# Kernel optimization log

Hardware: AMD Instinct MI355X
Metric: run time of the kernel (lower is better)

The kernel has to match this reference:

```python
import jax, jax.numpy as jnp
import numpy as np

D = 256          # in_dim == out_dim for both layers
B, S = 8, 1024   # batch, seq_len
EPS = 1e-5       # LayerNorm eps (torch default)


def _layernorm(x, g, b):
    mu = jnp.mean(x, axis=-1, keepdims=True)
    var = jnp.var(x, axis=-1, keepdims=True)
    return (x - mu) * jax.lax.rsqrt(var + EPS) * g + b


def _periods(d):
    i = jnp.arange(d, dtype=jnp.float32)
    # periods[i, j] = i*d + j + 2
    return i[:, None] * d + i[None, :] + 2.0


def _layer(x, M, P, g, b, positions):
    # x: [B, S, in_dim] -> [B, S, out_dim]
    x_trans = jnp.einsum('bsj,ij->bsi', x, M)      # x @ M.T
    x_trans = _layernorm(x_trans, g, b)
    k = positions.astype(jnp.float32)[:, None, None]            # [S,1,1]
    phi = jnp.cos(2.0 * jnp.pi * k / _periods(D)[None])         # [S,D,D]
    Mk = P[None] * phi                                          # [S,D,D]
    Nk = jnp.einsum('bsj,sij->bsi', x_trans, Mk)
    # use_residual='separate' with in_dim==out_dim -> Identity residual
    return Nk + x


def setup_inputs() -> dict:
    key = jax.random.key(0)
    ks = jax.random.split(key, 5)
    seq = jax.random.normal(ks[0], (B, S, D), dtype=jnp.float32)
    M1 = jax.random.uniform(ks[1], (D, D), jnp.float32, -0.5, 0.5)
    P1 = jax.random.uniform(ks[2], (D, D), jnp.float32, -0.1, 0.1)
    M2 = jax.random.uniform(ks[3], (D, D), jnp.float32, -0.5, 0.5)
    P2 = jax.random.uniform(ks[4], (D, D), jnp.float32, -0.1, 0.1)
    g1 = jnp.ones((D,), jnp.float32); b1 = jnp.zeros((D,), jnp.float32)
    g2 = jnp.ones((D,), jnp.float32); b2 = jnp.zeros((D,), jnp.float32)
    return {"seq": seq, "M1": M1, "P1": P1, "g1": g1, "b1": b1,
            "M2": M2, "P2": P2, "g2": g2, "b2": b2}


def reference(seq, M1, P1, g1, b1, M2, P2, g2, b2):
    positions = jnp.arange(S)
    x = _layer(seq, M1, P1, g1, b1, positions)
    x = _layer(x, M2, P2, g2, b2, positions)
    return x
```

## Files before the change

### kernel.cpp

```cpp
#include <hip/hip_runtime.h>

#define DD 256
#define BB 8
#define SS 1024
#define XSTRIDE 264
#define RSTRIDE 260

#define LAYER_BYTES 262144
#define PTAB_OFF    131072
#define WS_NEEDED   (2 * LAYER_BYTES)

typedef _Float16 half8  __attribute__((ext_vector_type(8)));
typedef _Float16 half2t __attribute__((ext_vector_type(2)));
typedef __fp16   fp16x2 __attribute__((ext_vector_type(2)));
typedef __attribute__((ext_vector_type(4))) float float4v;

union h8u { half8 h; half2t h2[4]; };

__device__ __forceinline__ half2t pkrtz(float a, float b) {
    union { fp16x2 f; half2t h; } cv;
    cv.f = __builtin_amdgcn_cvt_pkrtz(a, b);
    return cv.h;
}

__device__ __forceinline__ float cosrev(float x) {
    return __builtin_amdgcn_cosf(__builtin_amdgcn_fractf(x));
}
__device__ __forceinline__ float cosq(float x) {
    return __builtin_amdgcn_cosf(x);
}

__global__ void build_tabs(const float* __restrict__ M1, const float* __restrict__ P1,
                           const float* __restrict__ M2, const float* __restrict__ P2,
                           char* __restrict__ ws)
{
    int gid   = blockIdx.x * 256 + threadIdx.x;
    int layer = gid >> 13;
    int gi    = gid & 8191;
    int idx   = gi >> 6;
    int lane  = gi & 63;
    int wt    = idx & 15;
    int l15   = lane & 15, quad = lane >> 4;
    int kt    = idx >> 4;
    int n     = 16 * wt + l15;
    int j0    = kt * 32 + quad * 8;

    const float* Msrc = layer ? M2 : M1;
    const float* Psrc = layer ? P2 : P1;

    h8u mh, ph;
    #pragma unroll
    for (int e = 0; e < 4; ++e) {
        float ma = Msrc[(size_t)n * DD + j0 + 2 * e];
        float mb = Msrc[(size_t)n * DD + j0 + 2 * e + 1];
        float pa = Psrc[(size_t)n * DD + j0 + 2 * e];
        float pb = Psrc[(size_t)n * DD + j0 + 2 * e + 1];
        mh.h2[e] = pkrtz(ma, mb);
        ph.h2[e] = pkrtz(pa, pb);
    }
    char* base = ws + (size_t)layer * LAYER_BYTES;
    ((half8*)base)[gi]              = mh.h;
    ((half8*)(base + PTAB_OFF))[gi] = ph.h;
}

template<bool TABS>
__global__ __launch_bounds__(512, 8)
void fused_hierddpm(const float* __restrict__ seq,
                    const float* __restrict__ M1, const float* __restrict__ P1,
                    const float* __restrict__ g1, const float* __restrict__ be1,
                    const float* __restrict__ M2, const float* __restrict__ P2,
                    const float* __restrict__ g2, const float* __restrict__ be2,
                    const char* __restrict__ ws,
                    float* __restrict__ out)
{
    __shared__ __align__(16) _Float16 xsb[8][XSTRIDE];
    __shared__ __align__(16) _Float16 xtb[8][XSTRIDE];
    __shared__ __align__(16) float2 stats[8][8];
    __shared__ __align__(16) float res_lds[8][RSTRIDE];

    const int tid  = threadIdx.x;
    const int w    = tid >> 6;
    const int lane = tid & 63;
    const int l15  = lane & 15;
    const int l7   = l15 & 7;
    const int quad = lane >> 4;
    const int s    = blockIdx.x;
    const float k0 = (float)s;

    {
        const float4* seq4 = (const float4*)seq;
        int row = tid >> 6, j4 = tid & 63;
        float4 x = seq4[((size_t)row * SS + s) * 64 + j4];
        half2t* dst = (half2t*)&xsb[row][4 * j4];
        dst[0] = pkrtz(x.x, x.y);
        dst[1] = pkrtz(x.z, x.w);
        *(float4*)&res_lds[row][4 * j4] = x;
    }
    __syncthreads();

    #pragma unroll 1
    for (int layer = 0; layer < 2; ++layer) {
        const float* M  = layer ? M2  : M1;
        const float* P  = layer ? P2  : P1;
        const float* g  = layer ? g2  : g1;
        const float* be = layer ? be2 : be1;
        const char*  lbase = ws + (size_t)layer * LAYER_BYTES;
        const half8* Mtab = (const half8*)lbase;
        const half8* Ptab = (const half8*)(lbase + PTAB_OFF);

        float4v acc1[2];
        acc1[0] = (float4v){0.f, 0.f, 0.f, 0.f};
        acc1[1] = (float4v){0.f, 0.f, 0.f, 0.f};

        #pragma unroll 1
        for (int kt = 0; kt < 8; ++kt) {
            half8 a = *(const half8*)&xsb[l7][kt * 32 + quad * 8];
            #pragma unroll
            for (int t = 0; t < 2; ++t) {
                half8 bf;
                if (TABS) {
                    bf = Mtab[(kt * 16 + 2 * w + t) * 64 + lane];
                } else {
                    int n = 16 * (2 * w + t) + l15;
                    const float4* Mr = (const float4*)M + ((size_t)n * 64 + kt * 8 + quad * 2);
                    float4 m0 = Mr[0], m1 = Mr[1];
                    h8u bb2;
                    bb2.h2[0] = pkrtz(m0.x, m0.y);
                    bb2.h2[1] = pkrtz(m0.z, m0.w);
                    bb2.h2[2] = pkrtz(m1.x, m1.y);
                    bb2.h2[3] = pkrtz(m1.z, m1.w);
                    bf = bb2.h;
                }
                acc1[t] = __builtin_amdgcn_mfma_f32_16x16x32_f16(a, bf, acc1[t], 0, 0, 0);
            }
        }

        #pragma unroll
        for (int reg = 0; reg < 4; ++reg) {
            float v0 = acc1[0][reg], v1 = acc1[1][reg];
            float sm = v0 + v1;
            float sq = fmaf(v0, v0, v1 * v1);
            #pragma unroll
            for (int off = 1; off < 16; off <<= 1) {
                sm += __shfl_xor(sm, off, 64);
                sq += __shfl_xor(sq, off, 64);
            }
            if (l15 == 0 && quad < 2) stats[quad * 4 + reg][w] = make_float2(sm, sq);
        }
        __syncthreads();
        if (quad < 2) {
            int c0i = 16 * (2 * w) + l15, c1i = c0i + 16;
            float gv0 = g[c0i], bv0 = be[c0i];
            float gv1 = g[c1i], bv1 = be[c1i];
            #pragma unroll
            for (int reg = 0; reg < 4; ++reg) {
                int m = quad * 4 + reg;
                const float4* s4 = (const float4*)&stats[m][0];
                float4 q0 = s4[0], q1 = s4[1], q2 = s4[2], q3 = s4[3];
                float sm = (q0.x + q0.z) + (q1.x + q1.z) + (q2.x + q2.z) + (q3.x + q3.z);
                float sq = (q0.y + q0.w) + (q1.y + q1.w) + (q2.y + q2.w) + (q3.y + q3.w);
                float mm = sm * (1.f / DD);
                float rs = rsqrtf(sq * (1.f / DD) - mm * mm + 1e-5f);
                xtb[m][c0i] = (_Float16)fmaf((acc1[0][reg] - mm) * rs, gv0, bv0);
                xtb[m][c1i] = (_Float16)fmaf((acc1[1][reg] - mm) * rs, gv1, bv1);
            }
        }
        __syncthreads();

        float4v accS[2];
        accS[0] = (float4v){0.f, 0.f, 0.f, 0.f};
        accS[1] = (float4v){0.f, 0.f, 0.f, 0.f};

        float fb0 = (float)((16 * (2 * w) + l15) * DD + quad * 8 + 2);
        float fb1 = fb0 + 16.0f * DD;

        #pragma unroll 1
        for (int kt = 0; kt < 8; ++kt) {
            half8 a = *(const half8*)&xtb[l7][kt * 32 + quad * 8];
            {
                h8u pC;
                if (TABS) {
                    pC.h = Ptab[(kt * 16 + 2 * w) * 64 + lane];
                } else {
                    int n = 16 * (2 * w) + l15;
                    const float4* Pr = (const float4*)P + ((size_t)n * 64 + kt * 8 + quad * 2);
                    float4 p0 = Pr[0], p1 = Pr[1];
                    pC.h2[0] = pkrtz(p0.x, p0.y);
                    pC.h2[1] = pkrtz(p0.z, p0.w);
                    pC.h2[2] = pkrtz(p1.x, p1.y);
                    pC.h2[3] = pkrtz(p1.z, p1.w);
                }
                h8u bA;
                if (w == 0) {
                    #pragma unroll
                    for (int e = 0; e < 4; ++e) {
                        float ia = __builtin_amdgcn_rcpf(fb0 + (float)(2 * e));
                        float ib = __builtin_amdgcn_rcpf(fb0 + (float)(2 * e + 1));
                        bA.h2[e] = pC.h2[e] * pkrtz(cosrev(k0 * ia), cosrev(k0 * ib));
                    }
                } else {
                    #pragma unroll
                    for (int e = 0; e < 4; ++e) {
                        float ia = __builtin_amdgcn_rcpf(fb0 + (float)(2 * e));
                        float ib = __builtin_amdgcn_rcpf(fb0 + (float)(2 * e + 1));
                        bA.h2[e] = pC.h2[e] * pkrtz(cosq(k0 * ia), cosq(k0 * ib));
                    }
                }
                accS[0] = __builtin_amdgcn_mfma_f32_16x16x32_f16(a, bA.h, accS[0], 0, 0, 0);
                fb0 += 32.0f;
            }
            {
                h8u pC;
                if (TABS) {
                    pC.h = Ptab[(kt * 16 + 2 * w + 1) * 64 + lane];
                } else {
                    int n = 16 * (2 * w + 1) + l15;
                    const float4* Pr = (const float4*)P + ((size_t)n * 64 + kt * 8 + quad * 2);
                    float4 p0 = Pr[0], p1 = Pr[1];
                    pC.h2[0] = pkrtz(p0.x, p0.y);
                    pC.h2[1] = pkrtz(p0.z, p0.w);
                    pC.h2[2] = pkrtz(p1.x, p1.y);
                    pC.h2[3] = pkrtz(p1.z, p1.w);
                }
                h8u bB;
                #pragma unroll
                for (int e = 0; e < 4; ++e) {
                    float ia = __builtin_amdgcn_rcpf(fb1 + (float)(2 * e));
                    float ib = __builtin_amdgcn_rcpf(fb1 + (float)(2 * e + 1));
                    bB.h2[e] = pC.h2[e] * pkrtz(cosq(k0 * ia), cosq(k0 * ib));
                }
                accS[1] = __builtin_amdgcn_mfma_f32_16x16x32_f16(a, bB.h, accS[1], 0, 0, 0);
                fb1 += 32.0f;
            }
        }

        if (quad < 2) {
            #pragma unroll
            for (int t = 0; t < 2; ++t) {
                int col = 16 * (2 * w + t) + l15;
                #pragma unroll
                for (int reg = 0; reg < 4; ++reg) {
                    int m = quad * 4 + reg;
                    float val = accS[t][reg] + res_lds[m][col];
                    if (layer == 0) {
                        res_lds[m][col] = val;
                        xsb[m][col] = (_Float16)val;
                    } else {
                        out[((size_t)m * SS + s) * DD + col] = val;
                    }
                }
            }
        }
        if (layer == 0) __syncthreads();
    }
}

extern "C" void kernel_launch(void* const* d_in, const int* in_sizes, int n_in,
                              void* d_out, int out_size, void* d_ws, size_t ws_size,
                              hipStream_t stream)
{
    const float* seq = (const float*)d_in[0];
    const float* M1  = (const float*)d_in[1];
    const float* P1  = (const float*)d_in[2];
    const float* g1  = (const float*)d_in[3];
    const float* b1  = (const float*)d_in[4];
    const float* M2  = (const float*)d_in[5];
    const float* P2  = (const float*)d_in[6];
    const float* g2  = (const float*)d_in[7];
    const float* b2  = (const float*)d_in[8];
    float* out = (float*)d_out;

    if (ws_size >= WS_NEEDED) {
        build_tabs<<<64, 256, 0, stream>>>(M1, P1, M2, P2, (char*)d_ws);
        fused_hierddpm<true><<<SS, 512, 0, stream>>>(
            seq, M1, P1, g1, b1, M2, P2, g2, b2, (const char*)d_ws, out);
    } else {
        fused_hierddpm<false><<<SS, 512, 0, stream>>>(
            seq, M1, P1, g1, b1, M2, P2, g2, b2, nullptr, out);
    }
}
```

Measured before the change: 116.5 us.

## Precompute reciprocal period table and software-pipeline table loads in both GEMM loops

The prep kernel now also writes a float table of 1/period values for each layer, so the main kernel loads reciprocals instead of computing rcp on the fly. Both the M GEMM loop and the P-phase loop are double-buffered: next-iteration LDS and global table loads are issued before the current MFMAs. The first P/I tile loads are hoisted above the LayerNorm stats phase to hide latency. This trades rcp ALU work for extra global memory traffic (32 bytes per lane per tile) and higher register pressure, which could reduce occupancy under the 512x8 launch bounds.

```diff
diff --git a/kernel.cpp b/kernel.cpp
--- a/kernel.cpp
+++ b/kernel.cpp
@@ -6,8 +6,9 @@
 #define XSTRIDE 264
 #define RSTRIDE 260
 
-#define LAYER_BYTES 262144
+#define LAYER_BYTES 524288
 #define PTAB_OFF    131072
+#define ITAB_OFF    262144
 #define WS_NEEDED   (2 * LAYER_BYTES)
 
 typedef _Float16 half8  __attribute__((ext_vector_type(8)));
@@ -49,6 +50,7 @@
     const float* Psrc = layer ? P2 : P1;
 
     h8u mh, ph;
+    float iv[8];
     #pragma unroll
     for (int e = 0; e < 4; ++e) {
         float ma = Msrc[(size_t)n * DD + j0 + 2 * e];
@@ -57,10 +59,15 @@
         float pb = Psrc[(size_t)n * DD + j0 + 2 * e + 1];
         mh.h2[e] = pkrtz(ma, mb);
         ph.h2[e] = pkrtz(pa, pb);
+        iv[2 * e]     = 1.0f / (float)(n * DD + j0 + 2 * e + 2);
+        iv[2 * e + 1] = 1.0f / (float)(n * DD + j0 + 2 * e + 3);
     }
     char* base = ws + (size_t)layer * LAYER_BYTES;
     ((half8*)base)[gi]              = mh.h;
     ((half8*)(base + PTAB_OFF))[gi] = ph.h;
+    float4* it = (float4*)(base + ITAB_OFF);
+    it[2 * gi]     = make_float4(iv[0], iv[1], iv[2], iv[3]);
+    it[2 * gi + 1] = make_float4(iv[4], iv[5], iv[6], iv[7]);
 }
 
 template<bool TABS>
@@ -105,22 +112,35 @@
         const float* g  = layer ? g2  : g1;
         const float* be = layer ? be2 : be1;
         const char*  lbase = ws + (size_t)layer * LAYER_BYTES;
-        const half8* Mtab = (const half8*)lbase;
-        const half8* Ptab = (const half8*)(lbase + PTAB_OFF);
+        const half8*  Mtab = (const half8*)lbase;
+        const half8*  Ptab = (const half8*)(lbase + PTAB_OFF);
+        const float4* Itab = (const float4*)(lbase + ITAB_OFF);
 
         float4v acc1[2];
         acc1[0] = (float4v){0.f, 0.f, 0.f, 0.f};
         acc1[1] = (float4v){0.f, 0.f, 0.f, 0.f};
 
-        #pragma unroll 1
-        for (int kt = 0; kt < 8; ++kt) {
-            half8 a = *(const half8*)&xsb[l7][kt * 32 + quad * 8];
-            #pragma unroll
-            for (int t = 0; t < 2; ++t) {
-                half8 bf;
-                if (TABS) {
-                    bf = Mtab[(kt * 16 + 2 * w + t) * 64 + lane];
-                } else {
+        if (TABS) {
+            half8 aN  = *(const half8*)&xsb[l7][quad * 8];
+            half8 b0N = Mtab[(2 * w) * 64 + lane];
+            half8 b1N = Mtab[(2 * w + 1) * 64 + lane];
+            #pragma unroll 1
+            for (int kt = 0; kt < 8; ++kt) {
+                half8 aC = aN, b0C = b0N, b1C = b1N;
+                if (kt < 7) {
+                    aN  = *(const half8*)&xsb[l7][(kt + 1) * 32 + quad * 8];
+                    b0N = Mtab[((kt + 1) * 16 + 2 * w) * 64 + lane];
+                    b1N = Mtab[((kt + 1) * 16 + 2 * w + 1) * 64 + lane];
+                }
+                acc1[0] = __builtin_amdgcn_mfma_f32_16x16x32_f16(aC, b0C, acc1[0], 0, 0, 0);
+                acc1[1] = __builtin_amdgcn_mfma_f32_16x16x32_f16(aC, b1C, acc1[1], 0, 0, 0);
+            }
+        } else {
+            #pragma unroll 1
+            for (int kt = 0; kt < 8; ++kt) {
+                half8 a = *(const half8*)&xsb[l7][kt * 32 + quad * 8];
+                #pragma unroll
+                for (int t = 0; t < 2; ++t) {
                     int n = 16 * (2 * w + t) + l15;
                     const float4* Mr = (const float4*)M + ((size_t)n * 64 + kt * 8 + quad * 2);
                     float4 m0 = Mr[0], m1 = Mr[1];
@@ -129,10 +149,18 @@
                     bb2.h2[1] = pkrtz(m0.z, m0.w);
                     bb2.h2[2] = pkrtz(m1.x, m1.y);
                     bb2.h2[3] = pkrtz(m1.z, m1.w);
-                    bf = bb2.h;
-                }
-                acc1[t] = __builtin_amdgcn_mfma_f32_16x16x32_f16(a, bf, acc1[t], 0, 0, 0);
-            }
+                    acc1[t] = __builtin_amdgcn_mfma_f32_16x16x32_f16(a, bb2.h, acc1[t], 0, 0, 0);
+                }
+            }
+        }
+
+        half8 p0N, p1N;
+        float4 i0aN, i0bN, i1aN, i1bN;
+        if (TABS) {
+            int g0 = (2 * w) * 64 + lane, g1i = (2 * w + 1) * 64 + lane;
+            p0N = Ptab[g0];             p1N = Ptab[g1i];
+            i0aN = Itab[2 * g0];        i0bN = Itab[2 * g0 + 1];
+            i1aN = Itab[2 * g1i];       i1bN = Itab[2 * g1i + 1];
         }
 
         #pragma unroll
@@ -171,66 +199,75 @@
         accS[0] = (float4v){0.f, 0.f, 0.f, 0.f};
         accS[1] = (float4v){0.f, 0.f, 0.f, 0.f};
 
-        float fb0 = (float)((16 * (2 * w) + l15) * DD + quad * 8 + 2);
-        float fb1 = fb0 + 16.0f * DD;
-
-        #pragma unroll 1
-        for (int kt = 0; kt < 8; ++kt) {
-            half8 a = *(const half8*)&xtb[l7][kt * 32 + quad * 8];
-            {
-                h8u pC;
-                if (TABS) {
-                    pC.h = Ptab[(kt * 16 + 2 * w) * 64 + lane];
-                } else {
-                    int n = 16 * (2 * w) + l15;
+        if (TABS) {
+            half8 aN = *(const half8*)&xtb[l7][quad * 8];
+            #pragma unroll 1
+            for (int kt = 0; kt < 8; ++kt) {
+                half8 aC = aN;
+                h8u p0C, p1C;
+                p0C.h = p0N; p1C.h = p1N;
+                float4 i0a = i0aN, i0b = i0bN, i1a = i1aN, i1b = i1bN;
+                if (kt < 7) {
+                    int g0 = ((kt + 1) * 16 + 2 * w) * 64 + lane;
+                    int g1i = ((kt + 1) * 16 + 2 * w + 1) * 64 + lane;
+                    aN  = *(const half8*)&xtb[l7][(kt + 1) * 32 + quad * 8];
+                    p0N = Ptab[g0];        p1N = Ptab[g1i];
+                    i0aN = Itab[2 * g0];   i0bN = Itab[2 * g0 + 1];
+                    i1aN = Itab[2 * g1i];  i1bN = Itab[2 * g1i + 1];
+                }
+                {
+                    float iv[8] = {i0a.x, i0a.y, i0a.z, i0a.w, i0b.x, i0b.y, i0b.z, i0b.w};
+                    h8u bA;
+                    if (w == 0) {
+                        #pragma unroll
+                        for (int e = 0; e < 4; ++e)
+                            bA.h2[e] = p0C.h2[e] * pkrtz(cosrev(k0 * iv[2 * e]),
+                                                         cosrev(k0 * iv[2 * e + 1]));
+                    } else {
+                        #pragma unroll
+                        for (int e = 0; e < 4; ++e)
+                            bA.h2[e] = p0C.h2[e] * pkrtz(cosq(k0 * iv[2 * e]),
+                                                         cosq(k0 * iv[2 * e + 1]));
+                    }
+                    accS[0] = __builtin_amdgcn_mfma_f32_16x16x32_f16(aC, bA.h, accS[0], 0, 0, 0);
+                }
+                {
+                    float iv[8] = {i1a.x, i1a.y, i1a.z, i1a.w, i1b.x, i1b.y, i1b.z, i1b.w};
+                    h8u bB;
+                    #pragma unroll
+                    for (int e = 0; e < 4; ++e)
+                        bB.h2[e] = p1C.h2[e] * pkrtz(cosq(k0 * iv[2 * e]),
+                                                     cosq(k0 * iv[2 * e + 1]));
+                    accS[1] = __builtin_amdgcn_mfma_f32_16x16x32_f16(aC, bB.h, accS[1], 0, 0, 0);
+                }
+            }
+        } else {
+            float fb0 = (float)((16 * (2 * w) + l15) * DD + quad * 8 + 2);
+            float fb1 = fb0 + 16.0f * DD;
+            #pragma unroll 1
+            for (int kt = 0; kt < 8; ++kt) {
+                half8 a = *(const half8*)&xtb[l7][kt * 32 + quad * 8];
+                #pragma unroll
+                for (int t = 0; t < 2; ++t) {
+                    int n = 16 * (2 * w + t) + l15;
                     const float4* Pr = (const float4*)P + ((size_t)n * 64 + kt * 8 + quad * 2);
                     float4 p0 = Pr[0], p1 = Pr[1];
+                    h8u pC;
                     pC.h2[0] = pkrtz(p0.x, p0.y);
                     pC.h2[1] = pkrtz(p0.z, p0.w);
                     pC.h2[2] = pkrtz(p1.x, p1.y);
                     pC.h2[3] = pkrtz(p1.z, p1.w);
-                }
-                h8u bA;
-                if (w == 0) {
+                    float fb = (t == 0) ? fb0 : fb1;
+                    h8u bA;
                     #pragma unroll
                     for (int e = 0; e < 4; ++e) {
-                        float ia = __builtin_amdgcn_rcpf(fb0 + (float)(2 * e));
-                        float ib = __builtin_amdgcn_rcpf(fb0 + (float)(2 * e + 1));
+                        float ia = __builtin_amdgcn_rcpf(fb + (float)(2 * e));
+                        float ib = __builtin_amdgcn_rcpf(fb + (float)(2 * e + 1));
                         bA.h2[e] = pC.h2[e] * pkrtz(cosrev(k0 * ia), cosrev(k0 * ib));
                     }
-                } else {
-                    #pragma unroll
-                    for (int e = 0; e < 4; ++e) {
-                        float ia = __builtin_amdgcn_rcpf(fb0 + (float)(2 * e));
-                        float ib = __builtin_amdgcn_rcpf(fb0 + (float)(2 * e + 1));
-                        bA.h2[e] = pC.h2[e] * pkrtz(cosq(k0 * ia), cosq(k0 * ib));
-                    }
-                }
-                accS[0] = __builtin_amdgcn_mfma_f32_16x16x32_f16(a, bA.h, accS[0], 0, 0, 0);
-                fb0 += 32.0f;
-            }
-            {
-                h8u pC;
-                if (TABS) {
-                    pC.h = Ptab[(kt * 16 + 2 * w + 1) * 64 + lane];
-                } else {
-                    int n = 16 * (2 * w + 1) + l15;
-                    const float4* Pr = (const float4*)P + ((size_t)n * 64 + kt * 8 + quad * 2);
-                    float4 p0 = Pr[0], p1 = Pr[1];
-                    pC.h2[0] = pkrtz(p0.x, p0.y);
-                    pC.h2[1] = pkrtz(p0.z, p0.w);
-                    pC.h2[2] = pkrtz(p1.x, p1.y);
-                    pC.h2[3] = pkrtz(p1.z, p1.w);
-                }
-                h8u bB;
-                #pragma unroll
-                for (int e = 0; e < 4; ++e) {
-                    float ia = __builtin_amdgcn_rcpf(fb1 + (float)(2 * e));
-                    float ib = __builtin_amdgcn_rcpf(fb1 + (float)(2 * e + 1));
-                    bB.h2[e] = pC.h2[e] * pkrtz(cosq(k0 * ia), cosq(k0 * ib));
-                }
-                accS[1] = __builtin_amdgcn_mfma_f32_16x16x32_f16(a, bB.h, accS[1], 0, 0, 0);
-                fb1 += 32.0f;
+                    accS[t] = __builtin_amdgcn_mfma_f32_16x16x32_f16(a, bA.h, accS[t], 0, 0, 0);
+                }
+                fb0 += 32.0f; fb1 += 32.0f;
             }
         }
 
```

Result: slower. 285.8 us (+145.3%).
